# Kernel tuning notes

Measured on AMD Instinct MI355X. Metric: run time of the kernel, lower is better.

Reference implementation:

```python
import jax, jax.numpy as jnp
import numpy as np

C = 256
D = C // 8  # query/key channels


def setup_inputs() -> dict:
    key = jax.random.key(0)
    ks = jax.random.split(key, 7)
    x = jax.random.normal(ks[0], (4, C, 64, 64), dtype=jnp.float32)
    s1 = 1.0 / np.sqrt(C)
    w1 = jax.random.normal(ks[1], (D, C), dtype=jnp.float32) * s1
    b1 = jax.random.normal(ks[2], (D,), dtype=jnp.float32) * 0.01
    w2 = jax.random.normal(ks[3], (D, C), dtype=jnp.float32) * s1
    b2 = jax.random.normal(ks[4], (D,), dtype=jnp.float32) * 0.01
    w3 = jax.random.normal(ks[5], (C, C), dtype=jnp.float32) * s1
    b3 = jax.random.normal(ks[6], (C,), dtype=jnp.float32) * 0.01
    return {"x": x, "w1": w1, "b1": b1, "w2": w2, "b2": b2, "w3": w3, "b3": b3}


def reference(x, w1, b1, w2, b2, w3, b3):
    B, Cc, W, H = x.shape
    N = W * H
    xf = x.reshape(B, Cc, N)  # [B, C, N] flattened spatial
    # 1x1 convs are per-pixel linear maps over channels
    q = jnp.einsum('dc,bcn->bnd', w1, xf) + b1  # [B, N, D]
    k = jnp.einsum('dc,bcn->bdn', w2, xf) + b2[:, None]  # [B, D, N]
    v = jnp.einsum('oc,bcn->bon', w3, xf) + b3[:, None]  # [B, C, N]
    energy = jnp.einsum('bnd,bdm->bnm', q, k)  # [B, N, N]
    attn = jax.nn.softmax(energy, axis=-1)
    out = jnp.einsum('bcm,bnm->bcn', v, attn)  # bmm(V, attn^T)
    out = out.reshape(B, Cc, W, H) + x
    return out
```

## Files before the change

### kernel.cpp

```cpp
#include <hip/hip_runtime.h>
#include <hip/hip_fp16.h>

typedef _Float16 half8 __attribute__((ext_vector_type(8)));
typedef _Float16 half2v __attribute__((ext_vector_type(2)));
typedef float f32x16 __attribute__((ext_vector_type(16)));
typedef float f32x4v __attribute__((ext_vector_type(4)));

#define MFMA16(A, B, C) __builtin_amdgcn_mfma_f32_32x32x16_f16((A), (B), (C), 0, 0, 0)

__device__ __forceinline__ f32x16 fzero16() {
  f32x16 z;
#pragma unroll
  for (int i = 0; i < 16; ++i) z[i] = 0.0f;
  return z;
}

__device__ __forceinline__ float max16(float vm, const f32x16& s) {
  const float g1 = fmaxf(fmaxf(s[0], s[1]), s[2]);
  const float g2 = fmaxf(fmaxf(s[3], s[4]), s[5]);
  const float g3 = fmaxf(fmaxf(s[6], s[7]), s[8]);
  const float g4 = fmaxf(fmaxf(s[9], s[10]), s[11]);
  const float g5 = fmaxf(fmaxf(s[12], s[13]), s[14]);
  const float h1 = fmaxf(fmaxf(g1, g2), g3);
  const float h2 = fmaxf(fmaxf(g4, g5), s[15]);
  return fmaxf(fmaxf(vm, h1), h2);
}

__global__ __launch_bounds__(256) void wprep_kernel(
    const float* __restrict__ w1, const float* __restrict__ w2,
    const float* __restrict__ w3,
    _Float16* __restrict__ w1p, _Float16* __restrict__ w2p,
    _Float16* __restrict__ w3p)
{
  const int t = threadIdx.x;
  const int blk = blockIdx.x;
  if (blk < 32) {
    const int cot = blk >> 2, sub = blk & 3;
    for (int e = sub * 2048 + t; e < sub * 2048 + 2048; e += 256) {
      const int j = e & 7, l = (e >> 3) & 63, cs = e >> 9;
      const int lr = l & 31, h = l >> 5;
      const int row = cot * 32 + lr;
      const int col = cs * 16 + 4 * h + (j & 3) + 8 * (j >> 2);
      w3p[((cot * 16 + cs) * 64 + l) * 8 + j] = (_Float16)w3[row * 256 + col];
    }
  } else {
    const int sub = blk - 32;
    for (int e = sub * 1024 + t; e < sub * 1024 + 1024; e += 256) {
      const int j = e & 7, l = (e >> 3) & 63, cs = e >> 9;
      const int lr = l & 31, h = l >> 5;
      const int col = cs * 16 + 4 * h + (j & 3) + 8 * (j >> 2);
      const int idx = (cs * 64 + l) * 8 + j;
      w1p[idx] = (_Float16)w1[lr * 256 + col];
      w2p[idx] = (_Float16)w2[lr * 256 + col];
    }
  }
}

__global__ __launch_bounds__(256) void qkv_proj_kernel(
    const float* __restrict__ x,
    const _Float16* __restrict__ w1p, const float* __restrict__ b1,
    const _Float16* __restrict__ w2p, const float* __restrict__ b2,
    const _Float16* __restrict__ w3p, const float* __restrict__ b3,
    _Float16* __restrict__ qb, _Float16* __restrict__ kb,
    _Float16* __restrict__ vb)
{
  __shared__ f32x4v red[4][2][4][64];
  const int t = threadIdx.x, w = t >> 6, l = t & 63;
  const int lr = l & 31, h = l >> 5;
  const int b = blockIdx.x >> 7;
  const int nt = blockIdx.x & 127;
  const float* xb = x + (size_t)b * 256 * 4096 + nt * 32 + lr;
  const int cot0 = w * 2, cot1 = w * 2 + 1;

  f32x16 accq = fzero16(), acck = fzero16();
  f32x16 accv0 = fzero16(), accv1 = fzero16();

  for (int cs = 0; cs < 16; ++cs) {
    const int c0 = cs * 16 + 4 * h;
    half8 xh;
#pragma unroll
    for (int j = 0; j < 8; ++j) {
      const int c = c0 + (j & 3) + 8 * (j >> 2);
      xh[j] = (_Float16)xb[(size_t)c * 4096];
    }
    const half8 wh0 = *(const half8*)&w3p[((cot0 * 16 + cs) * 64 + l) * 8];
    const half8 wh1 = *(const half8*)&w3p[((cot1 * 16 + cs) * 64 + l) * 8];
    accv0 = MFMA16(xh, wh0, accv0);
    accv1 = MFMA16(xh, wh1, accv1);
    if ((cs >> 2) == w) {
      const half8 w1h = *(const half8*)&w1p[(cs * 64 + l) * 8];
      const half8 w2h = *(const half8*)&w2p[(cs * 64 + l) * 8];
      accq = MFMA16(w1h, xh, accq);
      acck = MFMA16(w2h, xh, acck);
    }
  }

  const float bv0 = b3[cot0 * 32 + lr];
  const float bv1 = b3[cot1 * 32 + lr];
#pragma unroll
  for (int hfq = 0; hfq < 2; ++hfq) {
    half8 p0, p1;
#pragma unroll
    for (int j = 0; j < 8; ++j) {
      p0[j] = (_Float16)(accv0[8 * hfq + j] + bv0);
      p1[j] = (_Float16)(accv1[8 * hfq + j] + bv1);
    }
    const int ms = nt * 2 + hfq;
    *(half8*)&vb[((((size_t)b * 256 + ms) * 8 + cot0) * 64 + l) * 8] = p0;
    *(half8*)&vb[((((size_t)b * 256 + ms) * 8 + cot1) * 64 + l) * 8] = p1;
  }

#pragma unroll
  for (int i4 = 0; i4 < 4; ++i4) {
    f32x4v q4, k4;
#pragma unroll
    for (int c = 0; c < 4; ++c) { q4[c] = accq[4 * i4 + c]; k4[c] = acck[4 * i4 + c]; }
    red[w][0][i4][l] = q4;
    red[w][1][i4][l] = k4;
  }
  __syncthreads();
  if (w < 2) {
    _Float16* dst = (w == 0) ? qb : kb;
    const float* bias = (w == 0) ? b1 : b2;
    f32x16 tot;
#pragma unroll
    for (int i4 = 0; i4 < 4; ++i4) {
      f32x4v v = red[0][w][i4][l];
      v += red[1][w][i4][l];
      v += red[2][w][i4][l];
      v += red[3][w][i4][l];
#pragma unroll
      for (int c = 0; c < 4; ++c) tot[4 * i4 + c] = v[c];
    }
#pragma unroll
    for (int ds = 0; ds < 2; ++ds) {
      half8 ph;
#pragma unroll
      for (int j = 0; j < 8; ++j) {
        const int d = 16 * ds + 4 * h + (j & 3) + 8 * (j >> 2);
        ph[j] = (_Float16)(tot[8 * ds + j] + bias[d]);
      }
      *(half8*)&dst[((((size_t)b * 128 + nt) * 2 + ds) * 64 + l) * 8] = ph;
    }
  }
}

__global__ __launch_bounds__(512, 1) void attn_kernel(
    const _Float16* __restrict__ qb, const _Float16* __restrict__ kb,
    const _Float16* __restrict__ vb,
    const float* __restrict__ x, float* __restrict__ out)
{
  __shared__ __align__(16) _Float16 Plds[2][2][2][8][64][8];
  __shared__ float Lred[2][4][32];
  const int t = threadIdx.x, w = t >> 6, l = t & 63;
  const int lr = l & 31, h = l >> 5;
  const int bid = blockIdx.x;
  const int xcd = bid & 7;
  const int b = xcd >> 1;
  const int rg = ((bid >> 3) << 1) | (xcd & 1);
  const int sw = w >> 2;
  const int kq = w & 3;

  const _Float16* kbase = kb + (size_t)b * 131072 + (size_t)l * 8;
  const _Float16* vbase = vb + (size_t)b * 1048576 + (size_t)w * 512 + (size_t)l * 8;

#define KF(kt, ds) (*(const half8*)(kbase + ((size_t)(((kt) * 4 + kq) * 2 + (ds))) * 512))
#define KFM(m, ds) (*(const half8*)(kbase + ((size_t)((m) * 2 + (ds))) * 512))
#define VF(kt, ks) (*(const half8*)(vbase + ((size_t)(((kt) * 8 + (ks)) * 8)) * 512))

  const int rt32q = rg * 2 + sw;
  const _Float16* qp = qb + (((size_t)b * 128 + rt32q) * 2 * 64 + l) * 8;
  const half8 qf0 = *(const half8*)qp;
  const half8 qf1 = *(const half8*)(qp + 512);
  const float LOG2E = 1.44269504088896340736f;

  f32x16 acc0 = fzero16(), acc1 = fzero16();
  float Lacc = 0.f;
  half8 va0[8], va1[8];
  half8 ka0, ka1, kb0_, kb1_;

#pragma unroll
  for (int ks = 0; ks < 8; ++ks) va0[ks] = VF(0, ks);
#pragma unroll
  for (int ks = 0; ks < 8; ++ks) va1[ks] = VF(1, ks);

  {
    float vm = -3.0e38f;
    for (int m = kq * 32; m < kq * 32 + 32; ++m) {
      const half8 k0 = KFM(m, 0);
      const half8 k1 = KFM(m, 1);
      f32x16 s = fzero16();
      s = MFMA16(k0, qf0, s);
      s = MFMA16(k1, qf1, s);
      vm = max16(vm, s);
    }
    vm = fmaxf(vm, __shfl_xor(vm, 32));
    if (l < 32) Lred[sw][kq][lr] = vm;
  }
  __syncthreads();
  const float Mr = fmaxf(fmaxf(Lred[sw][0][lr], Lred[sw][1][lr]),
                         fmaxf(Lred[sw][2][lr], Lred[sw][3][lr]));
  const float nM2 = -Mr * LOG2E;
  __syncthreads();

#define EXPPACK(S, BUF, TI)                                                    \
  {                                                                            \
    float pvv[16];                                                             \
    float ls = 0.f;                                                            \
    _Pragma("unroll") for (int i = 0; i < 16; ++i) {                           \
      pvv[i] = exp2f(fmaf((S)[i], LOG2E, nM2)); ls += pvv[i];                  \
    }                                                                          \
    Lacc += ls;                                                                \
    union { half8 v; half2v h2[4]; } u0, u1;                                   \
    _Pragma("unroll") for (int jj = 0; jj < 4; ++jj) {                         \
      auto a0 = __builtin_amdgcn_cvt_pkrtz(pvv[2 * jj], pvv[2 * jj + 1]);      \
      auto a1 = __builtin_amdgcn_cvt_pkrtz(pvv[8 + 2 * jj], pvv[8 + 2 * jj + 1]); \
      u0.h2[jj] = *(half2v*)&a0;                                               \
      u1.h2[jj] = *(half2v*)&a1;                                               \
    }                                                                          \
    *(half8*)&Plds[BUF][TI][sw][kq * 2 + 0][l][0] = u0.v;                      \
    *(half8*)&Plds[BUF][TI][sw][kq * 2 + 1][l][0] = u1.v;                      \
  }

#define PVC(CB, TI, VA)                                                        \
  {                                                                            \
    __builtin_amdgcn_s_setprio(1);                                             \
    _Pragma("unroll") for (int ks = 0; ks < 8; ++ks) {                         \
      const half8 pb0 = *(const half8*)&Plds[CB][TI][0][ks][l][0];             \
      const half8 pb1 = *(const half8*)&Plds[CB][TI][1][ks][l][0];             \
      acc0 = MFMA16(VA[ks], pb0, acc0);                                        \
      acc1 = MFMA16(VA[ks], pb1, acc1);                                        \
    }                                                                          \
    __builtin_amdgcn_s_setprio(0);                                             \
  }

  {
    const half8 k00 = KF(0, 0), k01 = KF(0, 1);
    f32x16 s = fzero16();
    s = MFMA16(k00, qf0, s);
    s = MFMA16(k01, qf1, s);
    ka0 = KF(2, 0); ka1 = KF(2, 1);
    EXPPACK(s, 0, 0)
  }
  {
    const half8 k10 = KF(1, 0), k11 = KF(1, 1);
    f32x16 s = fzero16();
    s = MFMA16(k10, qf0, s);
    s = MFMA16(k11, qf1, s);
    kb0_ = KF(3, 0); kb1_ = KF(3, 1);
    EXPPACK(s, 0, 1)
  }
  asm volatile("s_waitcnt lgkmcnt(0)" ::: "memory");
  __builtin_amdgcn_s_barrier();
  asm volatile("" ::: "memory");

  for (int P = 0; P < 16; ++P) {
    const int CB = P & 1, PB = CB ^ 1;
    const int p0 = 2 * P + 2, p1 = 2 * P + 3;

    if (p0 < 32) {
      f32x16 s = fzero16();
      s = MFMA16(ka0, qf0, s);
      s = MFMA16(ka1, qf1, s);
      if (p0 + 2 < 32) { ka0 = KF(p0 + 2, 0); ka1 = KF(p0 + 2, 1); }
      EXPPACK(s, PB, 0)
    }
    PVC(CB, 0, va0)
    if (p0 < 32) {
#pragma unroll
      for (int ks = 0; ks < 8; ++ks) va0[ks] = VF(p0, ks);
    }

    if (p1 < 32) {
      f32x16 s = fzero16();
      s = MFMA16(kb0_, qf0, s);
      s = MFMA16(kb1_, qf1, s);
      if (p1 + 2 < 32) { kb0_ = KF(p1 + 2, 0); kb1_ = KF(p1 + 2, 1); }
      EXPPACK(s, PB, 1)
    }
    PVC(CB, 1, va1)
    if (p1 < 32) {
#pragma unroll
      for (int ks = 0; ks < 8; ++ks) va1[ks] = VF(p1, ks);
    }

    asm volatile("s_waitcnt lgkmcnt(0)" ::: "memory");
    __builtin_amdgcn_s_barrier();
    asm volatile("" ::: "memory");
  }
#undef PVC
#undef EXPPACK
#undef KF
#undef KFM
#undef VF

  {
    const float l2 = Lacc + __shfl_xor(Lacc, 32);
    if (l < 32) Lred[sw][kq][lr] = l2;
  }
  __syncthreads();
  const float invL0 = 1.0f / (Lred[0][0][lr] + Lred[0][1][lr] + Lred[0][2][lr] + Lred[0][3][lr]);
  const float invL1 = 1.0f / (Lred[1][0][lr] + Lred[1][1][lr] + Lred[1][2][lr] + Lred[1][3][lr]);

  const float* xb = x + (size_t)b * 1048576;
  float* ob = out + (size_t)b * 1048576;
  const int nn0 = rg * 64 + lr;
  const int nn1 = rg * 64 + 32 + lr;
#pragma unroll
  for (int reg = 0; reg < 16; ++reg) {
    const int crel = (reg & 3) + 8 * (reg >> 2) + 4 * h;
    const int cout = w * 32 + crel;
    const size_t o0 = (size_t)cout * 4096 + nn0;
    ob[o0] = acc0[reg] * invL0 + xb[o0];
    const size_t o1 = (size_t)cout * 4096 + nn1;
    ob[o1] = acc1[reg] * invL1 + xb[o1];
  }
}

extern "C" void kernel_launch(void* const* d_in, const int* in_sizes, int n_in,
                              void* d_out, int out_size, void* d_ws, size_t ws_size,
                              hipStream_t stream) {
  const float* x  = (const float*)d_in[0];
  const float* w1 = (const float*)d_in[1];
  const float* b1 = (const float*)d_in[2];
  const float* w2 = (const float*)d_in[3];
  const float* b2 = (const float*)d_in[4];
  const float* w3 = (const float*)d_in[5];
  const float* b3 = (const float*)d_in[6];
  float* out = (float*)d_out;

  char* ws = (char*)d_ws;
  _Float16* qb  = (_Float16*)(ws);
  _Float16* kb  = (_Float16*)(ws + (1u << 20));
  _Float16* vb  = (_Float16*)(ws + (2u << 20));
  _Float16* w1p = (_Float16*)(ws + (10u << 20) + (64u << 10));
  _Float16* w2p = (_Float16*)(ws + (10u << 20) + (96u << 10));
  _Float16* w3p = (_Float16*)(ws + (10u << 20) + (128u << 10));

  hipLaunchKernelGGL(wprep_kernel, dim3(40), dim3(256), 0, stream,
                     w1, w2, w3, w1p, w2p, w3p);
  hipLaunchKernelGGL(qkv_proj_kernel, dim3(512), dim3(256), 0, stream,
                     x, w1p, b1, w2p, b2, w3p, b3, qb, kb, vb);
  hipLaunchKernelGGL(attn_kernel, dim3(256), dim3(512), 0, stream,
                     qb, kb, vb, x, out);
}
```

Baseline: 76.22 us.

## Split attention into 32-row query tiles across twice as many blocks

```diff
diff --git a/kernel.cpp b/kernel.cpp
--- a/kernel.cpp
+++ b/kernel.cpp
@@ -145,65 +145,65 @@
   }
 }
 
-__global__ __launch_bounds__(512, 1) void attn_kernel(
+__global__ __launch_bounds__(512, 4) void attn_kernel(
     const _Float16* __restrict__ qb, const _Float16* __restrict__ kb,
     const _Float16* __restrict__ vb,
     const float* __restrict__ x, float* __restrict__ out)
 {
-  __shared__ __align__(16) _Float16 Plds[2][2][2][8][64][8];
-  __shared__ float Lred[2][4][32];
+  __shared__ __align__(16) _Float16 Plds[2][2][8][64][8];
+  __shared__ float Lred[8][32];
   const int t = threadIdx.x, w = t >> 6, l = t & 63;
   const int lr = l & 31, h = l >> 5;
   const int bid = blockIdx.x;
   const int xcd = bid & 7;
   const int b = xcd >> 1;
   const int rg = ((bid >> 3) << 1) | (xcd & 1);
-  const int sw = w >> 2;
-  const int kq = w & 3;
+  const int ti = w >> 2;
+  const int qq = w & 3;
 
   const _Float16* kbase = kb + (size_t)b * 131072 + (size_t)l * 8;
   const _Float16* vbase = vb + (size_t)b * 1048576 + (size_t)w * 512 + (size_t)l * 8;
 
-#define KF(kt, ds) (*(const half8*)(kbase + ((size_t)(((kt) * 4 + kq) * 2 + (ds))) * 512))
 #define KFM(m, ds) (*(const half8*)(kbase + ((size_t)((m) * 2 + (ds))) * 512))
-#define VF(kt, ks) (*(const half8*)(vbase + ((size_t)(((kt) * 8 + (ks)) * 8)) * 512))
-
-  const int rt32q = rg * 2 + sw;
-  const _Float16* qp = qb + (((size_t)b * 128 + rt32q) * 2 * 64 + l) * 8;
+#define VF(P, TI, ks) (*(const half8*)(vbase + ((size_t)(16 * (P) + 8 * (TI) + (ks))) * 4096))
+
+  const _Float16* qp = qb + (((size_t)b * 128 + rg) * 2 * 64 + l) * 8;
   const half8 qf0 = *(const half8*)qp;
   const half8 qf1 = *(const half8*)(qp + 512);
   const float LOG2E = 1.44269504088896340736f;
 
-  f32x16 acc0 = fzero16(), acc1 = fzero16();
+  f32x16 acc = fzero16();
   float Lacc = 0.f;
   half8 va0[8], va1[8];
-  half8 ka0, ka1, kb0_, kb1_;
-
-#pragma unroll
-  for (int ks = 0; ks < 8; ++ks) va0[ks] = VF(0, ks);
-#pragma unroll
-  for (int ks = 0; ks < 8; ++ks) va1[ks] = VF(1, ks);
+  half8 kc0, kc1;
+
+#pragma unroll
+  for (int ks = 0; ks < 8; ++ks) va0[ks] = VF(0, 0, ks);
+#pragma unroll
+  for (int ks = 0; ks < 8; ++ks) va1[ks] = VF(0, 1, ks);
 
   {
     float vm = -3.0e38f;
-    for (int m = kq * 32; m < kq * 32 + 32; ++m) {
-      const half8 k0 = KFM(m, 0);
-      const half8 k1 = KFM(m, 1);
+    half8 sk0 = KFM(16 * w, 0), sk1 = KFM(16 * w, 1);
+    for (int m = 16 * w; m < 16 * w + 16; ++m) {
+      half8 nk0, nk1;
+      if (m + 1 < 16 * w + 16) { nk0 = KFM(m + 1, 0); nk1 = KFM(m + 1, 1); }
       f32x16 s = fzero16();
-      s = MFMA16(k0, qf0, s);
-      s = MFMA16(k1, qf1, s);
+      s = MFMA16(sk0, qf0, s);
+      s = MFMA16(sk1, qf1, s);
       vm = max16(vm, s);
+      sk0 = nk0; sk1 = nk1;
     }
     vm = fmaxf(vm, __shfl_xor(vm, 32));
-    if (l < 32) Lred[sw][kq][lr] = vm;
+    if (l < 32) Lred[w][lr] = vm;
   }
   __syncthreads();
-  const float Mr = fmaxf(fmaxf(Lred[sw][0][lr], Lred[sw][1][lr]),
-                         fmaxf(Lred[sw][2][lr], Lred[sw][3][lr]));
+  float Mr = Lred[0][lr];
+#pragma unroll
+  for (int ww = 1; ww < 8; ++ww) Mr = fmaxf(Mr, Lred[ww][lr]);
   const float nM2 = -Mr * LOG2E;
-  __syncthreads();
-
-#define EXPPACK(S, BUF, TI)                                                    \
+
+#define EXPPACK(S, BUF)                                                        \
   {                                                                            \
     float pvv[16];                                                             \
     float ls = 0.f;                                                            \
@@ -218,37 +218,27 @@
       u0.h2[jj] = *(half2v*)&a0;                                               \
       u1.h2[jj] = *(half2v*)&a1;                                               \
     }                                                                          \
-    *(half8*)&Plds[BUF][TI][sw][kq * 2 + 0][l][0] = u0.v;                      \
-    *(half8*)&Plds[BUF][TI][sw][kq * 2 + 1][l][0] = u1.v;                      \
+    *(half8*)&Plds[BUF][ti][qq * 2 + 0][l][0] = u0.v;                          \
+    *(half8*)&Plds[BUF][ti][qq * 2 + 1][l][0] = u1.v;                          \
   }
 
 #define PVC(CB, TI, VA)                                                        \
   {                                                                            \
     __builtin_amdgcn_s_setprio(1);                                             \
     _Pragma("unroll") for (int ks = 0; ks < 8; ++ks) {                         \
-      const half8 pb0 = *(const half8*)&Plds[CB][TI][0][ks][l][0];             \
-      const half8 pb1 = *(const half8*)&Plds[CB][TI][1][ks][l][0];             \
-      acc0 = MFMA16(VA[ks], pb0, acc0);                                        \
-      acc1 = MFMA16(VA[ks], pb1, acc1);                                        \
+      const half8 pb = *(const half8*)&Plds[CB][TI][ks][l][0];                 \
+      acc = MFMA16(VA[ks], pb, acc);                                           \
     }                                                                          \
     __builtin_amdgcn_s_setprio(0);                                             \
   }
 
+  kc0 = KFM(w, 0); kc1 = KFM(w, 1);
   {
-    const half8 k00 = KF(0, 0), k01 = KF(0, 1);
     f32x16 s = fzero16();
-    s = MFMA16(k00, qf0, s);
-    s = MFMA16(k01, qf1, s);
-    ka0 = KF(2, 0); ka1 = KF(2, 1);
-    EXPPACK(s, 0, 0)
-  }
-  {
-    const half8 k10 = KF(1, 0), k11 = KF(1, 1);
-    f32x16 s = fzero16();
-    s = MFMA16(k10, qf0, s);
-    s = MFMA16(k11, qf1, s);
-    kb0_ = KF(3, 0); kb1_ = KF(3, 1);
-    EXPPACK(s, 0, 1)
+    s = MFMA16(kc0, qf0, s);
+    s = MFMA16(kc1, qf1, s);
+    kc0 = KFM(8 + w, 0); kc1 = KFM(8 + w, 1);
+    EXPPACK(s, 0)
   }
   asm volatile("s_waitcnt lgkmcnt(0)" ::: "memory");
   __builtin_amdgcn_s_barrier();
@@ -256,32 +246,23 @@
 
   for (int P = 0; P < 16; ++P) {
     const int CB = P & 1, PB = CB ^ 1;
-    const int p0 = 2 * P + 2, p1 = 2 * P + 3;
-
-    if (p0 < 32) {
+
+    if (P + 1 < 16) {
       f32x16 s = fzero16();
-      s = MFMA16(ka0, qf0, s);
-      s = MFMA16(ka1, qf1, s);
-      if (p0 + 2 < 32) { ka0 = KF(p0 + 2, 0); ka1 = KF(p0 + 2, 1); }
-      EXPPACK(s, PB, 0)
+      s = MFMA16(kc0, qf0, s);
+      s = MFMA16(kc1, qf1, s);
+      if (P + 2 < 16) { kc0 = KFM(8 * (P + 2) + w, 0); kc1 = KFM(8 * (P + 2) + w, 1); }
+      EXPPACK(s, PB)
     }
     PVC(CB, 0, va0)
-    if (p0 < 32) {
-#pragma unroll
-      for (int ks = 0; ks < 8; ++ks) va0[ks] = VF(p0, ks);
-    }
-
-    if (p1 < 32) {
-      f32x16 s = fzero16();
-      s = MFMA16(kb0_, qf0, s);
-      s = MFMA16(kb1_, qf1, s);
-      if (p1 + 2 < 32) { kb0_ = KF(p1 + 2, 0); kb1_ = KF(p1 + 2, 1); }
-      EXPPACK(s, PB, 1)
+    if (P + 1 < 16) {
+#pragma unroll
+      for (int ks = 0; ks < 8; ++ks) va0[ks] = VF(P + 1, 0, ks);
     }
     PVC(CB, 1, va1)
-    if (p1 < 32) {
-#pragma unroll
-      for (int ks = 0; ks < 8; ++ks) va1[ks] = VF(p1, ks);
+    if (P + 1 < 16) {
+#pragma unroll
+      for (int ks = 0; ks < 8; ++ks) va1[ks] = VF(P + 1, 1, ks);
     }
 
     asm volatile("s_waitcnt lgkmcnt(0)" ::: "memory");
@@ -290,30 +271,28 @@
   }
 #undef PVC
 #undef EXPPACK
-#undef KF
 #undef KFM
 #undef VF
 
   {
     const float l2 = Lacc + __shfl_xor(Lacc, 32);
-    if (l < 32) Lred[sw][kq][lr] = l2;
+    if (l < 32) Lred[w][lr] = l2;
   }
   __syncthreads();
-  const float invL0 = 1.0f / (Lred[0][0][lr] + Lred[0][1][lr] + Lred[0][2][lr] + Lred[0][3][lr]);
-  const float invL1 = 1.0f / (Lred[1][0][lr] + Lred[1][1][lr] + Lred[1][2][lr] + Lred[1][3][lr]);
+  float Ls = Lred[0][lr];
+#pragma unroll
+  for (int ww = 1; ww < 8; ++ww) Ls += Lred[ww][lr];
+  const float invL = 1.0f / Ls;
 
   const float* xb = x + (size_t)b * 1048576;
   float* ob = out + (size_t)b * 1048576;
-  const int nn0 = rg * 64 + lr;
-  const int nn1 = rg * 64 + 32 + lr;
+  const int nn = rg * 32 + lr;
 #pragma unroll
   for (int reg = 0; reg < 16; ++reg) {
     const int crel = (reg & 3) + 8 * (reg >> 2) + 4 * h;
     const int cout = w * 32 + crel;
-    const size_t o0 = (size_t)cout * 4096 + nn0;
-    ob[o0] = acc0[reg] * invL0 + xb[o0];
-    const size_t o1 = (size_t)cout * 4096 + nn1;
-    ob[o1] = acc1[reg] * invL1 + xb[o1];
+    const size_t o = (size_t)cout * 4096 + nn;
+    ob[o] = acc[reg] * invL + xb[o];
   }
 }
 
@@ -341,6 +320,6 @@
                      w1, w2, w3, w1p, w2p, w3p);
   hipLaunchKernelGGL(qkv_proj_kernel, dim3(512), dim3(256), 0, stream,
                      x, w1p, b1, w2p, b2, w3p, b3, qb, kb, vb);
-  hipLaunchKernelGGL(attn_kernel, dim3(256), dim3(512), 0, stream,
+  hipLaunchKernelGGL(attn_kernel, dim3(512), dim3(512), 0, stream,
                      qb, kb, vb, x, out);
 }
```

Result: slower. 82.96 us (+8.8%).
